# Optimization experiments

Measured on AMD Instinct MI355X. Metric: run time of the kernel, lower is better.

Reference implementation:

```python
import jax, jax.numpy as jnp
import numpy as np

EMB = 1024
HEADS = EMB // 64  # 16, head_dim = 64


def setup_inputs() -> dict:
    key = jax.random.key(0)
    ks = jax.random.split(key, 9)
    a, m, t, e = 4, 2048, 2048, EMB
    s = 1.0 / np.sqrt(e)
    return {
        "q": jax.random.normal(ks[0], (a, m, e), jnp.float32),
        "k": jax.random.normal(ks[1], (a, t, e), jnp.float32),
        "v": jax.random.normal(ks[2], (a, t, e), jnp.float32),
        "Wq": jax.random.normal(ks[3], (e, e), jnp.float32) * s,
        "bq": jnp.zeros((e,), jnp.float32),
        "Wk": jax.random.normal(ks[4], (e, e), jnp.float32) * s,
        "bk": jnp.zeros((e,), jnp.float32),
        "Wv": jax.random.normal(ks[5], (e, e), jnp.float32) * s,
        "bv": jnp.zeros((e,), jnp.float32),
    }


def reference(q, k, v, Wq, bq, Wk, bk, Wv, bv):
    a, m, e = q.shape
    t = k.shape[1]
    h = HEADS
    # linear projections (torch Linear: x @ W.T + b)
    qp = (q @ Wq.T + bq).reshape(a, m, h, -1).transpose(0, 2, 1, 3)  # [a,h,m,c]
    kp = (k @ Wk.T + bk).reshape(a, t, h, -1).transpose(0, 2, 1, 3)  # [a,h,t,c]
    vp = (v @ Wv.T + bv).reshape(a, t, h, -1).transpose(0, 2, 1, 3)  # [a,h,t,c]
    # NOTE: original forward never applies self.scale — unscaled QK^T (faithful)
    dots = jnp.einsum('ahmc,ahtc->ahmt', qp, kp)
    attn = jax.nn.softmax(dots, axis=-1)
    out = jnp.einsum('ahmt,ahtc->ahmc', attn, vp)
    return out.transpose(0, 2, 1, 3).reshape(a, m, e)
```

## Files before the change

### kernel.cpp

```cpp
#include <hip/hip_runtime.h>
#include <hip/hip_bf16.h>
#include <hip/hip_fp16.h>

using half8  = __attribute__((ext_vector_type(8))) _Float16;
using float4v = __attribute__((ext_vector_type(4))) float;
using f32x16 = __attribute__((ext_vector_type(16))) float;
typedef unsigned int uint;

#define A_DIM 4
#define M_DIM 2048
#define E_DIM 1024
#define H_DIM 16
#define C_DIM 64
#define PLANE (M_DIM * C_DIM)
#define PROJ_ELEMS (A_DIM * H_DIM * PLANE)
#define LOG2E 1.44269504088896f

#define GLOAD_LDS16(g, l) __builtin_amdgcn_global_load_lds( \
    (const __attribute__((address_space(1))) void*)(g), \
    (__attribute__((address_space(3))) void*)(l), 16, 0, 0)

#if __has_builtin(__builtin_amdgcn_exp2f)
#define EXP2F(x) __builtin_amdgcn_exp2f(x)
#else
#define EXP2F(x) exp2f(x)
#endif

static __device__ __forceinline__ uint pk16(float a, float b) {
    auto r = __builtin_amdgcn_cvt_pkrtz(a, b);
    return __builtin_bit_cast(uint, r);
}

static __device__ __forceinline__ half8 ldsfrag_cvt256(const float* base, int row, int colbyte) {
    const char* b = (const char*)base;
    int off = row * 256 + (colbyte ^ ((row & 7) << 4));
    float4v x0 = *reinterpret_cast<const float4v*>(b + off);
    float4v x1 = *reinterpret_cast<const float4v*>(b + (off ^ 16));
    union { uint u[4]; half8 v; } r;
    r.u[0] = pk16(x0[0], x0[1]);
    r.u[1] = pk16(x0[2], x0[3]);
    r.u[2] = pk16(x1[0], x1[1]);
    r.u[3] = pk16(x1[2], x1[3]);
    return r.v;
}

__global__ __launch_bounds__(256)
void wcvt_kernel(const float* __restrict__ Wq, const float* __restrict__ Wk,
                 const float* __restrict__ Wv, _Float16* __restrict__ wh)
{
    const float* W = (blockIdx.y == 0) ? Wq : (blockIdx.y == 1) ? Wk : Wv;
    _Float16* o = wh + (size_t)blockIdx.y * E_DIM * E_DIM;
    int i = (blockIdx.x * 256 + threadIdx.x) * 8;
    float4v x0 = *reinterpret_cast<const float4v*>(&W[i]);
    float4v x1 = *reinterpret_cast<const float4v*>(&W[i + 4]);
    union { uint u[4]; half8 h; } r;
    r.u[0] = pk16(x0[0], x0[1]);
    r.u[1] = pk16(x0[2], x0[3]);
    r.u[2] = pk16(x1[0], x1[1]);
    r.u[3] = pk16(x1[2], x1[3]);
    *reinterpret_cast<half8*>(&o[i]) = r.h;
}

template<int MODE>
__global__ __launch_bounds__(256, 3)
void proj_kernel(const float* __restrict__ X, const _Float16* __restrict__ Wh,
                 const float* __restrict__ bias, _Float16* __restrict__ out)
{
    __shared__ float    ldsA[128 * 64];
    __shared__ _Float16 ldsB[128 * 64];

    const int tid  = threadIdx.x;
    const int lane = tid & 63;
    const int wave = tid >> 6;
    const int wr = wave >> 1, wc = wave & 1;
    const int g = lane >> 4, r16 = lane & 15;
    const int R0 = blockIdx.x * 128;
    const int C0 = blockIdx.y * 128;

    float4v acc[4][4];
#pragma unroll
    for (int i = 0; i < 4; i++)
#pragma unroll
        for (int j = 0; j < 4; j++) acc[i][j] = {0.f, 0.f, 0.f, 0.f};

    for (int k0 = 0; k0 < E_DIM; k0 += 64) {
        __syncthreads();
#pragma unroll
        for (int i = 0; i < 8; i++) {
            int s    = i * 256 + tid;
            int row  = s >> 4;
            int swzo = ((s & 15) * 16) ^ ((row & 7) << 4);
            const char* asrc = (const char*)&X[(size_t)(R0 + row) * E_DIM + k0] + swzo;
            GLOAD_LDS16(asrc, &ldsA[s * 4]);
        }
#pragma unroll
        for (int i = 0; i < 4; i++) {
            int s    = i * 256 + tid;
            int row  = s >> 3;
            int swzo = ((s & 7) * 16) ^ ((row & 7) << 4);
            const char* bsrc = (const char*)&Wh[(size_t)(C0 + row) * E_DIM + k0] + swzo;
            GLOAD_LDS16(bsrc, &ldsB[s * 8]);
        }
        __syncthreads();

#pragma unroll
        for (int kc = 0; kc < 2; kc++) {
            half8 af[4], bf[4];
#pragma unroll
            for (int mi = 0; mi < 4; mi++)
                af[mi] = ldsfrag_cvt256(ldsA, wr * 64 + mi * 16 + r16, kc * 128 + g * 32);
#pragma unroll
            for (int ni = 0; ni < 4; ni++) {
                int row = wc * 64 + ni * 16 + r16;
                bf[ni] = *reinterpret_cast<const half8*>(
                    (const char*)ldsB + row * 128 + ((kc * 64 + g * 16) ^ ((row & 7) << 4)));
            }
#pragma unroll
            for (int mi = 0; mi < 4; mi++)
#pragma unroll
                for (int ni = 0; ni < 4; ni++)
                    acc[mi][ni] = __builtin_amdgcn_mfma_f32_16x16x32_f16(af[mi], bf[ni], acc[mi][ni], 0, 0, 0);
        }
    }

#pragma unroll
    for (int mi = 0; mi < 4; mi++) {
#pragma unroll
        for (int ni = 0; ni < 4; ni++) {
            const int jb = C0 + wc * 64 + ni * 16 + r16;
            const int h  = jb >> 6;
            const int cc = jb & 63;
            const float bv = bias[jb];
            if (MODE == 0) {
#pragma unroll
                for (int reg = 0; reg < 4; reg++) {
                    int b = R0 + wr * 64 + mi * 16 + g * 4 + reg;
                    float val = acc[mi][ni][reg] + bv;
                    size_t o = (size_t)((b >> 11) * H_DIM + h) * PLANE + (size_t)(b & (M_DIM - 1)) * C_DIM + cc;
                    out[o] = (_Float16)val;
                }
            } else {
                int b0 = R0 + wr * 64 + mi * 16 + g * 4;
                uint u0 = pk16(acc[mi][ni][0] + bv, acc[mi][ni][1] + bv);
                uint u1 = pk16(acc[mi][ni][2] + bv, acc[mi][ni][3] + bv);
                size_t o = (size_t)((b0 >> 11) * H_DIM + h) * PLANE + (size_t)cc * M_DIM + (b0 & (M_DIM - 1));
                *reinterpret_cast<uint*>(&out[o]) = u0;
                *reinterpret_cast<uint*>(&out[o] + 2) = u1;
            }
        }
    }
}

__global__ __launch_bounds__(256, 4)
void flash_kernel(const _Float16* __restrict__ qp, const _Float16* __restrict__ kp,
                  const _Float16* __restrict__ vt, float* __restrict__ out)
{
    __shared__ _Float16 smem[2][2][4096];

    const int tid  = threadIdx.x;
    const int lane = tid & 63;
    const int wave = tid >> 6;
    const int l31  = lane & 31;
    const int hi   = lane >> 5;

    const int bid = blockIdx.x;
    const int wg  = ((bid & 7) << 7) | (bid >> 3);
    const int plane_i = wg >> 4;
    const int qt      = wg & 15;
    const size_t plane = (size_t)plane_i * PLANE;
    const int q0 = qt * 128 + wave * 32;

    const int srow  = tid >> 3;
    const int lincb = (tid & 7) * 16;
    const int scb   = lincb ^ ((srow & 7) << 4);

    half8 qf[4];
#pragma unroll
    for (int ch = 0; ch < 4; ch++)
        qf[ch] = *reinterpret_cast<const half8*>(&qp[plane + (size_t)(q0 + l31) * C_DIM + ch * 16 + hi * 8]);

    f32x16 o0, o1;
#pragma unroll
    for (int i = 0; i < 16; i++) { o0[i] = 0.f; o1[i] = 0.f; }
    float m = 0.f, mK = 0.f, l = 0.f;

    auto stage = [&](int buf, int t0) {
#pragma unroll
        for (int i = 0; i < 2; i++) {
            int row = srow + 32 * i;
            const char* ksrc = (const char*)&kp[plane + (size_t)(t0 + row) * C_DIM] + scb;
            const char* vsrc = (const char*)&vt[plane + (size_t)row * M_DIM + t0] + scb;
            GLOAD_LDS16(ksrc, &smem[buf][0][tid * 8 + 2048 * i]);
            GLOAD_LDS16(vsrc, &smem[buf][1][tid * 8 + 2048 * i]);
        }
    };

    stage(0, 0);

    for (int it = 0; it < M_DIM / 64; ++it) {
        __syncthreads();
        if (it + 1 < M_DIM / 64) stage((it + 1) & 1, (it + 1) * 64);
        const int cur = it & 1;
        const char* kbase = (const char*)smem[cur][0];
        const char* vbase = (const char*)smem[cur][1];

#pragma unroll
        for (int st = 0; st < 2; ++st) {
            const int krow = st * 32 + l31;
            const int kswz = (krow & 7) << 4;
            f32x16 s;
#pragma unroll
            for (int i = 0; i < 16; i++) s[i] = 0.f;
            __builtin_amdgcn_s_setprio(1);
#pragma unroll
            for (int ch = 0; ch < 4; ch++) {
                int cb = (ch * 32 + hi * 16) ^ kswz;
                half8 kf = *reinterpret_cast<const half8*>(kbase + krow * 128 + cb);
                s = __builtin_amdgcn_mfma_f32_32x32x16_f16(kf, qf[ch], s, 0, 0, 0);
            }
            __builtin_amdgcn_s_setprio(0);

            float p[16];
#pragma unroll
            for (int r = 0; r < 16; r++) p[r] = EXP2F(fmaf(s[r], LOG2E, -mK));

            float a0 = fmaxf(fmaxf(s[0],  s[1]),  s[2]);
            float a1 = fmaxf(fmaxf(s[3],  s[4]),  s[5]);
            float a2 = fmaxf(fmaxf(s[6],  s[7]),  s[8]);
            float a3 = fmaxf(fmaxf(s[9],  s[10]), s[11]);
            float a4 = fmaxf(fmaxf(s[12], s[13]), s[14]);
            float pm = fmaxf(fmaxf(fmaxf(a0, a1), a2),
                             fmaxf(fmaxf(a3, a4), s[15]));
            pm = fmaxf(pm, __shfl_xor(pm, 32));
            if (!__all(pm <= m + 8.f)) {
                float mnew = fmaxf(m, pm);
                float sc = EXP2F((m - mnew) * LOG2E);
                m = mnew; mK = m * LOG2E;
                l *= sc;
                o0 *= sc; o1 *= sc;
#pragma unroll
                for (int r = 0; r < 16; r++) p[r] *= sc;
            }
            float t0a = (p[0] + p[1]) + (p[2] + p[3]);
            float t1a = (p[4] + p[5]) + (p[6] + p[7]);
            float t2a = (p[8] + p[9]) + (p[10] + p[11]);
            float t3a = (p[12] + p[13]) + (p[14] + p[15]);
            l += (t0a + t1a) + (t2a + t3a);

            half8 pf[2];
#pragma unroll
            for (int c0 = 0; c0 < 2; c0++) {
                uint ua0 = pk16(p[8 * c0 + 0], p[8 * c0 + 1]);
                uint ua1 = pk16(p[8 * c0 + 2], p[8 * c0 + 3]);
                uint ub0 = pk16(p[8 * c0 + 4], p[8 * c0 + 5]);
                uint ub1 = pk16(p[8 * c0 + 6], p[8 * c0 + 7]);
                union { int u[4]; half8 v; } pu;
#if __has_builtin(__builtin_amdgcn_permlane32_swap)
                auto r0 = __builtin_amdgcn_permlane32_swap((int)ua0, (int)ub0, false, false);
                auto r1 = __builtin_amdgcn_permlane32_swap((int)ua1, (int)ub1, false, false);
                pu.u[0] = r0[0];
                pu.u[1] = r1[0];
                pu.u[2] = r0[1];
                pu.u[3] = r1[1];
#else
                uint v0 = hi ? ua0 : ub0;
                uint v1 = hi ? ua1 : ub1;
                uint y0 = (uint)__shfl_xor((int)v0, 32);
                uint y1 = (uint)__shfl_xor((int)v1, 32);
                pu.u[0] = hi ? y0 : ua0;
                pu.u[1] = hi ? y1 : ua1;
                pu.u[2] = hi ? ub0 : y0;
                pu.u[3] = hi ? ub1 : y1;
#endif
                pf[c0] = pu.v;
            }

            __builtin_amdgcn_s_setprio(1);
#pragma unroll
            for (int db = 0; db < 2; db++) {
                const int vrow = db * 32 + l31;
                const int vswz = (vrow & 7) << 4;
#pragma unroll
                for (int c0 = 0; c0 < 2; c0++) {
                    int cb = (st * 64 + c0 * 32 + hi * 16) ^ vswz;
                    half8 vf = *reinterpret_cast<const half8*>(vbase + vrow * 128 + cb);
                    if (db == 0) o0 = __builtin_amdgcn_mfma_f32_32x32x16_f16(vf, pf[c0], o0, 0, 0, 0);
                    else         o1 = __builtin_amdgcn_mfma_f32_32x32x16_f16(vf, pf[c0], o1, 0, 0, 0);
                }
            }
            __builtin_amdgcn_s_setprio(0);
        }
    }

    const int aa = plane_i >> 4;
    const int hh = plane_i & 15;
    const float lt = l + __shfl_xor(l, 32);
    const float inv = 1.f / lt;
    float* obase = out + ((size_t)(aa * M_DIM + q0 + l31)) * E_DIM + hh * C_DIM;
#pragma unroll
    for (int db = 0; db < 2; db++) {
#pragma unroll
        for (int g4 = 0; g4 < 4; g4++) {
            float4v w;
#pragma unroll
            for (int j = 0; j < 4; j++) w[j] = (db ? o1[4 * g4 + j] : o0[4 * g4 + j]) * inv;
            int d0 = db * 32 + 8 * g4 + 4 * hi;
            *reinterpret_cast<float4v*>(obase + d0) = w;
        }
    }
}

extern "C" void kernel_launch(void* const* d_in, const int* in_sizes, int n_in,
                              void* d_out, int out_size, void* d_ws, size_t ws_size,
                              hipStream_t stream)
{
    const float* q  = (const float*)d_in[0];
    const float* k  = (const float*)d_in[1];
    const float* v  = (const float*)d_in[2];
    const float* Wq = (const float*)d_in[3];
    const float* bq = (const float*)d_in[4];
    const float* Wk = (const float*)d_in[5];
    const float* bk = (const float*)d_in[6];
    const float* Wv = (const float*)d_in[7];
    const float* bv = (const float*)d_in[8];
    float* out = (float*)d_out;

    _Float16* qp = (_Float16*)d_ws;
    _Float16* kp = qp + PROJ_ELEMS;
    _Float16* vt = kp + PROJ_ELEMS;

    const size_t e2 = (size_t)E_DIM * E_DIM;
    const size_t need_bytes = ((size_t)PROJ_ELEMS * 3 + 3 * e2) * sizeof(_Float16);
    _Float16* wh = (ws_size >= need_bytes) ? (vt + PROJ_ELEMS) : (_Float16*)d_out;

    hipLaunchKernelGGL(wcvt_kernel, dim3(512, 3), dim3(256), 0, stream, Wq, Wk, Wv, wh);

    dim3 pg(64, 8), pb(256);
    hipLaunchKernelGGL((proj_kernel<0>), pg, pb, 0, stream, q, wh,          bq, qp);
    hipLaunchKernelGGL((proj_kernel<0>), pg, pb, 0, stream, k, wh + e2,     bk, kp);
    hipLaunchKernelGGL((proj_kernel<1>), pg, pb, 0, stream, v, wh + 2 * e2, bv, vt);
    hipLaunchKernelGGL(flash_kernel, dim3(A_DIM * H_DIM * (M_DIM / 128)), dim3(256), 0, stream, qp, kp, vt, out);
}
```

Before: 195.7 us.

## Process two 32-row query tiles per wave to reuse K/V LDS reads

Each wave of the flash attention kernel now handles 64 query rows (two 32-row sub-tiles) instead of 32, so each workgroup covers 256 queries and the grid halves. K and V fragments read from LDS are reused across both query sub-tiles, halving LDS and global K/V traffic per query and giving the scheduler two independent MFMA chains. In exchange, register pressure roughly doubles for accumulators, launch bounds drop to 2 blocks per CU, and there are fewer workgroups (512) to fill the GPU.

```diff
diff --git a/kernel.cpp b/kernel.cpp
--- a/kernel.cpp
+++ b/kernel.cpp
@@ -151,7 +151,7 @@
     }
 }
 
-__global__ __launch_bounds__(256, 4)
+__global__ __launch_bounds__(256, 2)
 void flash_kernel(const _Float16* __restrict__ qp, const _Float16* __restrict__ kp,
                   const _Float16* __restrict__ vt, float* __restrict__ out)
 {
@@ -164,25 +164,28 @@
     const int hi   = lane >> 5;
 
     const int bid = blockIdx.x;
-    const int wg  = ((bid & 7) << 7) | (bid >> 3);
-    const int plane_i = wg >> 4;
-    const int qt      = wg & 15;
+    const int wg  = ((bid & 7) << 6) | (bid >> 3);
+    const int plane_i = wg >> 3;
+    const int qt      = wg & 7;
     const size_t plane = (size_t)plane_i * PLANE;
-    const int q0 = qt * 128 + wave * 32;
+    const int q0 = qt * 256 + wave * 64;
 
     const int srow  = tid >> 3;
     const int lincb = (tid & 7) * 16;
     const int scb   = lincb ^ ((srow & 7) << 4);
 
-    half8 qf[4];
-#pragma unroll
-    for (int ch = 0; ch < 4; ch++)
-        qf[ch] = *reinterpret_cast<const half8*>(&qp[plane + (size_t)(q0 + l31) * C_DIM + ch * 16 + hi * 8]);
-
-    f32x16 o0, o1;
-#pragma unroll
-    for (int i = 0; i < 16; i++) { o0[i] = 0.f; o1[i] = 0.f; }
-    float m = 0.f, mK = 0.f, l = 0.f;
+    half8 qf0[4], qf1[4];
+#pragma unroll
+    for (int ch = 0; ch < 4; ch++) {
+        qf0[ch] = *reinterpret_cast<const half8*>(&qp[plane + (size_t)(q0 + l31) * C_DIM + ch * 16 + hi * 8]);
+        qf1[ch] = *reinterpret_cast<const half8*>(&qp[plane + (size_t)(q0 + 32 + l31) * C_DIM + ch * 16 + hi * 8]);
+    }
+
+    f32x16 o00, o01, o10, o11;
+#pragma unroll
+    for (int i = 0; i < 16; i++) { o00[i] = 0.f; o01[i] = 0.f; o10[i] = 0.f; o11[i] = 0.f; }
+    float m0 = 0.f, mK0 = 0.f, l0 = 0.f;
+    float m1 = 0.f, mK1 = 0.f, l1 = 0.f;
 
     auto stage = [&](int buf, int t0) {
 #pragma unroll
@@ -208,71 +211,87 @@
         for (int st = 0; st < 2; ++st) {
             const int krow = st * 32 + l31;
             const int kswz = (krow & 7) << 4;
-            f32x16 s;
-#pragma unroll
-            for (int i = 0; i < 16; i++) s[i] = 0.f;
+
+            half8 kf[4];
+#pragma unroll
+            for (int ch = 0; ch < 4; ch++)
+                kf[ch] = *reinterpret_cast<const half8*>(kbase + krow * 128 + ((ch * 32 + hi * 16) ^ kswz));
+
+            f32x16 s0, s1;
+#pragma unroll
+            for (int i = 0; i < 16; i++) { s0[i] = 0.f; s1[i] = 0.f; }
             __builtin_amdgcn_s_setprio(1);
 #pragma unroll
             for (int ch = 0; ch < 4; ch++) {
-                int cb = (ch * 32 + hi * 16) ^ kswz;
-                half8 kf = *reinterpret_cast<const half8*>(kbase + krow * 128 + cb);
-                s = __builtin_amdgcn_mfma_f32_32x32x16_f16(kf, qf[ch], s, 0, 0, 0);
+                s0 = __builtin_amdgcn_mfma_f32_32x32x16_f16(kf[ch], qf0[ch], s0, 0, 0, 0);
+                s1 = __builtin_amdgcn_mfma_f32_32x32x16_f16(kf[ch], qf1[ch], s1, 0, 0, 0);
             }
             __builtin_amdgcn_s_setprio(0);
 
-            float p[16];
-#pragma unroll
-            for (int r = 0; r < 16; r++) p[r] = EXP2F(fmaf(s[r], LOG2E, -mK));
-
-            float a0 = fmaxf(fmaxf(s[0],  s[1]),  s[2]);
-            float a1 = fmaxf(fmaxf(s[3],  s[4]),  s[5]);
-            float a2 = fmaxf(fmaxf(s[6],  s[7]),  s[8]);
-            float a3 = fmaxf(fmaxf(s[9],  s[10]), s[11]);
-            float a4 = fmaxf(fmaxf(s[12], s[13]), s[14]);
-            float pm = fmaxf(fmaxf(fmaxf(a0, a1), a2),
-                             fmaxf(fmaxf(a3, a4), s[15]));
-            pm = fmaxf(pm, __shfl_xor(pm, 32));
-            if (!__all(pm <= m + 8.f)) {
-                float mnew = fmaxf(m, pm);
-                float sc = EXP2F((m - mnew) * LOG2E);
-                m = mnew; mK = m * LOG2E;
-                l *= sc;
-                o0 *= sc; o1 *= sc;
-#pragma unroll
-                for (int r = 0; r < 16; r++) p[r] *= sc;
-            }
-            float t0a = (p[0] + p[1]) + (p[2] + p[3]);
-            float t1a = (p[4] + p[5]) + (p[6] + p[7]);
-            float t2a = (p[8] + p[9]) + (p[10] + p[11]);
-            float t3a = (p[12] + p[13]) + (p[14] + p[15]);
-            l += (t0a + t1a) + (t2a + t3a);
-
-            half8 pf[2];
-#pragma unroll
-            for (int c0 = 0; c0 < 2; c0++) {
-                uint ua0 = pk16(p[8 * c0 + 0], p[8 * c0 + 1]);
-                uint ua1 = pk16(p[8 * c0 + 2], p[8 * c0 + 3]);
-                uint ub0 = pk16(p[8 * c0 + 4], p[8 * c0 + 5]);
-                uint ub1 = pk16(p[8 * c0 + 6], p[8 * c0 + 7]);
-                union { int u[4]; half8 v; } pu;
+            half8 pf0[2], pf1[2];
+#pragma unroll
+            for (int qh = 0; qh < 2; qh++) {
+                f32x16& s = qh ? s1 : s0;
+                float& m = qh ? m1 : m0;
+                float& mK = qh ? mK1 : mK0;
+                float& l = qh ? l1 : l0;
+                half8* pf = qh ? pf1 : pf0;
+                f32x16& oa = qh ? o10 : o00;
+                f32x16& ob = qh ? o11 : o01;
+
+                float p[16];
+#pragma unroll
+                for (int r = 0; r < 16; r++) p[r] = EXP2F(fmaf(s[r], LOG2E, -mK));
+
+                float a0 = fmaxf(fmaxf(s[0],  s[1]),  s[2]);
+                float a1 = fmaxf(fmaxf(s[3],  s[4]),  s[5]);
+                float a2 = fmaxf(fmaxf(s[6],  s[7]),  s[8]);
+                float a3 = fmaxf(fmaxf(s[9],  s[10]), s[11]);
+                float a4 = fmaxf(fmaxf(s[12], s[13]), s[14]);
+                float pm = fmaxf(fmaxf(fmaxf(a0, a1), a2),
+                                 fmaxf(fmaxf(a3, a4), s[15]));
+                pm = fmaxf(pm, __shfl_xor(pm, 32));
+                if (!__all(pm <= m + 8.f)) {
+                    float mnew = fmaxf(m, pm);
+                    float sc = EXP2F((m - mnew) * LOG2E);
+                    m = mnew; mK = m * LOG2E;
+                    l *= sc;
+                    oa *= sc; ob *= sc;
+#pragma unroll
+                    for (int r = 0; r < 16; r++) p[r] *= sc;
+                }
+                float t0a = (p[0] + p[1]) + (p[2] + p[3]);
+                float t1a = (p[4] + p[5]) + (p[6] + p[7]);
+                float t2a = (p[8] + p[9]) + (p[10] + p[11]);
+                float t3a = (p[12] + p[13]) + (p[14] + p[15]);
+                l += (t0a + t1a) + (t2a + t3a);
+
+#pragma unroll
+                for (int c0 = 0; c0 < 2; c0++) {
+                    uint ua0 = pk16(p[8 * c0 + 0], p[8 * c0 + 1]);
+                    uint ua1 = pk16(p[8 * c0 + 2], p[8 * c0 + 3]);
+                    uint ub0 = pk16(p[8 * c0 + 4], p[8 * c0 + 5]);
+                    uint ub1 = pk16(p[8 * c0 + 6], p[8 * c0 + 7]);
+                    union { int u[4]; half8 v; } pu;
 #if __has_builtin(__builtin_amdgcn_permlane32_swap)
-                auto r0 = __builtin_amdgcn_permlane32_swap((int)ua0, (int)ub0, false, false);
-                auto r1 = __builtin_amdgcn_permlane32_swap((int)ua1, (int)ub1, false, false);
-                pu.u[0] = r0[0];
-                pu.u[1] = r1[0];
-                pu.u[2] = r0[1];
-                pu.u[3] = r1[1];
+                    auto r0 = __builtin_amdgcn_permlane32_swap((int)ua0, (int)ub0, false, false);
+                    auto r1 = __builtin_amdgcn_permlane32_swap((int)ua1, (int)ub1, false, false);
+                    pu.u[0] = r0[0];
+                    pu.u[1] = r1[0];
+                    pu.u[2] = r0[1];
+                    pu.u[3] = r1[1];
 #else
-                uint v0 = hi ? ua0 : ub0;
-                uint v1 = hi ? ua1 : ub1;
-                uint y0 = (uint)__shfl_xor((int)v0, 32);
-                uint y1 = (uint)__shfl_xor((int)v1, 32);
-                pu.u[0] = hi ? y0 : ua0;
-                pu.u[1] = hi ? y1 : ua1;
-                pu.u[2] = hi ? ub0 : y0;
-                pu.u[3] = hi ? ub1 : y1;
+                    uint v0 = hi ? ua0 : ub0;
+                    uint v1 = hi ? ua1 : ub1;
+                    uint y0 = (uint)__shfl_xor((int)v0, 32);
+                    uint y1 = (uint)__shfl_xor((int)v1, 32);
+                    pu.u[0] = hi ? y0 : ua0;
+                    pu.u[1] = hi ? y1 : ua1;
+                    pu.u[2] = hi ? ub0 : y0;
+                    pu.u[3] = hi ? ub1 : y1;
 #endif
-                pf[c0] = pu.v;
+                    pf[c0] = pu.v;
+                }
             }
 
             __builtin_amdgcn_s_setprio(1);
@@ -282,10 +301,15 @@
                 const int vswz = (vrow & 7) << 4;
 #pragma unroll
                 for (int c0 = 0; c0 < 2; c0++) {
-                    int cb = (st * 64 + c0 * 32 + hi * 16) ^ vswz;
-                    half8 vf = *reinterpret_cast<const half8*>(vbase + vrow * 128 + cb);
-                    if (db == 0) o0 = __builtin_amdgcn_mfma_f32_32x32x16_f16(vf, pf[c0], o0, 0, 0, 0);
-                    else         o1 = __builtin_amdgcn_mfma_f32_32x32x16_f16(vf, pf[c0], o1, 0, 0, 0);
+                    half8 vf = *reinterpret_cast<const half8*>(
+                        vbase + vrow * 128 + ((st * 64 + c0 * 32 + hi * 16) ^ vswz));
+                    if (db == 0) {
+                        o00 = __builtin_amdgcn_mfma_f32_32x32x16_f16(vf, pf0[c0], o00, 0, 0, 0);
+                        o10 = __builtin_amdgcn_mfma_f32_32x32x16_f16(vf, pf1[c0], o10, 0, 0, 0);
+                    } else {
+                        o01 = __builtin_amdgcn_mfma_f32_32x32x16_f16(vf, pf0[c0], o01, 0, 0, 0);
+                        o11 = __builtin_amdgcn_mfma_f32_32x32x16_f16(vf, pf1[c0], o11, 0, 0, 0);
+                    }
                 }
             }
             __builtin_amdgcn_s_setprio(0);
@@ -294,18 +318,23 @@
 
     const int aa = plane_i >> 4;
     const int hh = plane_i & 15;
-    const float lt = l + __shfl_xor(l, 32);
-    const float inv = 1.f / lt;
-    float* obase = out + ((size_t)(aa * M_DIM + q0 + l31)) * E_DIM + hh * C_DIM;
-#pragma unroll
-    for (int db = 0; db < 2; db++) {
-#pragma unroll
-        for (int g4 = 0; g4 < 4; g4++) {
-            float4v w;
-#pragma unroll
-            for (int j = 0; j < 4; j++) w[j] = (db ? o1[4 * g4 + j] : o0[4 * g4 + j]) * inv;
-            int d0 = db * 32 + 8 * g4 + 4 * hi;
-            *reinterpret_cast<float4v*>(obase + d0) = w;
+#pragma unroll
+    for (int qh = 0; qh < 2; qh++) {
+        float lown = qh ? l1 : l0;
+        const float lt = lown + __shfl_xor(lown, 32);
+        const float inv = 1.f / lt;
+        float* obase = out + ((size_t)(aa * M_DIM + q0 + qh * 32 + l31)) * E_DIM + hh * C_DIM;
+#pragma unroll
+        for (int db = 0; db < 2; db++) {
+            const f32x16& ov = qh ? (db ? o11 : o10) : (db ? o01 : o00);
+#pragma unroll
+            for (int g4 = 0; g4 < 4; g4++) {
+                float4v w;
+#pragma unroll
+                for (int j = 0; j < 4; j++) w[j] = ov[4 * g4 + j] * inv;
+                int d0 = db * 32 + 8 * g4 + 4 * hi;
+                *reinterpret_cast<float4v*>(obase + d0) = w;
+            }
         }
     }
 }
@@ -339,5 +368,5 @@
     hipLaunchKernelGGL((proj_kernel<0>), pg, pb, 0, stream, q, wh,          bq, qp);
     hipLaunchKernelGGL((proj_kernel<0>), pg, pb, 0, stream, k, wh + e2,     bk, kp);
     hipLaunchKernelGGL((proj_kernel<1>), pg, pb, 0, stream, v, wh + 2 * e2, bv, vt);
-    hipLaunchKernelGGL(flash_kernel, dim3(A_DIM * H_DIM * (M_DIM / 128)), dim3(256), 0, stream, qp, kp, vt, out);
-}
+    hipLaunchKernelGGL(flash_kernel, dim3(A_DIM * H_DIM * (M_DIM / 256)), dim3(256), 0, stream, qp, kp, vt, out);
+}
```

Result: faster. 182.9 us (-6.5%).
